# Kernel optimization log

Hardware: AMD Instinct MI355X
Metric: run time of the kernel (lower is better)

The kernel has to match this reference:

```python
import jax, jax.numpy as jnp
import numpy as np


def setup_inputs() -> dict:
    key = jax.random.key(0)
    k_x, k_w, k_s, k_b = jax.random.split(key, 4)
    B, S, D_IN, D_OUT = 8, 2048, 4096, 4096
    x = jax.random.normal(k_x, (B, S, D_IN), dtype=jnp.float32)
    # int8-valued weights stored as int32 (values in [-128, 127])
    quantized_weights = jax.random.randint(k_w, (D_OUT, D_IN), -128, 128, dtype=jnp.int32)
    scales = jax.random.normal(k_s, (D_OUT,), dtype=jnp.float32)
    bias = jax.random.normal(k_b, (D_OUT,), dtype=jnp.float32)
    return {"x": x, "quantized_weights": quantized_weights, "scales": scales, "bias": bias}


def reference(x, quantized_weights, scales, bias):
    # Per-output-channel dequant: W[o, i] = q[o, i] * scales[o]
    dequantized_weight = quantized_weights.astype(x.dtype) * scales[:, None].astype(x.dtype)
    # F.linear: y = x @ W^T + b
    return jnp.einsum('bsi,oi->bso', x, dequantized_weight) + bias.astype(x.dtype)
```

## Files before the change

kernel.cpp:

```cpp
#include <hip/hip_runtime.h>

#define M_DIM 16384
#define N_DIM 4096
#define K_DIM 4096
#define NT 32

typedef __attribute__((ext_vector_type(4))) float f32x4;
typedef __attribute__((ext_vector_type(8))) short bf16x8;
typedef __attribute__((ext_vector_type(4))) int i32x4;

__device__ __forceinline__ short f2bf(float f) {
    unsigned int u = __builtin_bit_cast(unsigned int, f);
    u += 0x7FFFu + ((u >> 16) & 1u);
    return (short)(u >> 16);
}

__global__ __launch_bounds__(256)
void quant_x_kernel(const float* __restrict__ x, char* __restrict__ x8,
                    float* __restrict__ rs) {
    const int row = blockIdx.x;
    const int tid = threadIdx.x;
    const float* xr = x + (size_t)row * K_DIM;
    f32x4 v[4];
    float am = 0.f;
#pragma unroll
    for (int p = 0; p < 4; ++p) {
        v[p] = *(const f32x4*)(xr + p * 1024 + tid * 4);
#pragma unroll
        for (int e = 0; e < 4; ++e) am = fmaxf(am, fabsf(v[p][e]));
    }
#pragma unroll
    for (int off = 32; off >= 1; off >>= 1)
        am = fmaxf(am, __shfl_xor(am, off, 64));
    __shared__ float smax[4];
    if ((tid & 63) == 0) smax[tid >> 6] = am;
    __syncthreads();
    am = fmaxf(fmaxf(smax[0], smax[1]), fmaxf(smax[2], smax[3]));
    const float inv = am > 0.f ? 127.f / am : 0.f;
    if (tid == 0) rs[row] = am / 127.f;
    int* o32 = (int*)(x8 + (size_t)row * K_DIM);
#pragma unroll
    for (int p = 0; p < 4; ++p) {
        const int b0 = (int)rintf(v[p][0] * inv);
        const int b1 = (int)rintf(v[p][1] * inv);
        const int b2 = (int)rintf(v[p][2] * inv);
        const int b3 = (int)rintf(v[p][3] * inv);
        o32[p * 256 + tid] = (b0 & 255) | ((b1 & 255) << 8) | ((b2 & 255) << 16) | ((b3 & 255) << 24);
    }
}

__global__ void quant_w_kernel(const int* __restrict__ q, char* __restrict__ w8, long n) {
    long i = ((long)blockIdx.x * blockDim.x + threadIdx.x) * 16;
    const long stride = (long)gridDim.x * blockDim.x * 16;
    for (; i < n; i += stride) {
        i32x4 o;
#pragma unroll
        for (int j = 0; j < 4; ++j) {
            i32x4 a = *(const i32x4*)(q + i + j * 4);
            o[j] = (a[0] & 255) | ((a[1] & 255) << 8) | ((a[2] & 255) << 16) | ((a[3] & 255) << 24);
        }
        *(i32x4*)(w8 + i) = o;
    }
}

__device__ __forceinline__ void load_lds16(const void* g, void* l) {
    __builtin_amdgcn_global_load_lds((const __attribute__((address_space(1))) void*)g,
                                     (__attribute__((address_space(3))) void*)l, 16, 0, 0);
}

#define BAR() __builtin_amdgcn_s_barrier()
#define VM(n) asm volatile("s_waitcnt vmcnt(" #n ")" ::: "memory")

__global__ __launch_bounds__(512, 2)
void gemm8p_i8(const char* __restrict__ A, const char* __restrict__ Bw,
               const float* __restrict__ rs, const float* __restrict__ scales,
               const float* __restrict__ bias, float* __restrict__ out) {
    __shared__ char lds[2][4][128 * 128];

    const int tid  = threadIdx.x;
    const int lane = tid & 63;
    const int w    = tid >> 6;
    const int wm   = w >> 2;
    const int wn   = w & 3;
    const int lrow = lane & 15;
    const int lkg  = lane >> 4;
    const int sx   = lane & 7;

    const int nwg = gridDim.x;
    const int swz = (blockIdx.x & 7) * (nwg >> 3) + (blockIdx.x >> 3);
    const int bn  = (swz & 15) * 256;
    const int bm  = (swz >> 4) * 256;

    const char* aS[2];
    const char* bS[2];
#pragma unroll
    for (int L = 0; L < 2; ++L) {
        const int c   = L * 512 + tid;
        const int row = c >> 3;
        const int kc  = (c & 7) ^ (row & 7);
        const int mA  = bm + ((row >> 6) << 7) + (row & 63);
        const int nB  = bn + ((row >> 5) << 6) + (row & 31);
        aS[L] = A  + (size_t)mA * K_DIM + kc * 16;
        bS[L] = Bw + (size_t)nB * K_DIM + kc * 16;
    }
    const int wofs = w << 10;

#define STAGE_A(buf, q, kt) do { \
    char* d = &lds[buf][q][wofs]; \
    const long ko = (long)(kt) * 128 + (long)(q) * (64 * (long)K_DIM); \
    load_lds16(aS[0] + ko, d); \
    load_lds16(aS[1] + ko, d + 8192); \
} while (0)

#define STAGE_B(buf, nh, kt) do { \
    char* d = &lds[buf][2 + (nh)][wofs]; \
    const long ko = (long)(kt) * 128 + (long)(nh) * (32 * (long)K_DIM); \
    load_lds16(bS[0] + ko, d); \
    load_lds16(bS[1] + ko, d + 8192); \
} while (0)

    const int aoff = (wm << 6) + lrow;
    const int boff = (wn << 5) + lrow;

#define RD_A(buf, q, sub, ks) \
    (*(const i32x4*)&lds[buf][q][((aoff + (sub) * 16) << 7) + (((((ks) << 2) + lkg) ^ sx) << 4)])
#define RD_B(buf, nh, sub, ks) \
    (*(const i32x4*)&lds[buf][2 + (nh)][((boff + (sub) * 16) << 7) + (((((ks) << 2) + lkg) ^ sx) << 4)])

    i32x4 acc[8][4];
#pragma unroll
    for (int i = 0; i < 8; ++i)
#pragma unroll
        for (int j = 0; j < 4; ++j)
            acc[i][j] = (i32x4){0, 0, 0, 0};

    i32x4 aF[4][2], bF0[2][2], bF1[2][2];

#define LOAD_AF(buf, q) do { \
    _Pragma("unroll") for (int ii = 0; ii < 4; ++ii) { \
        aF[ii][0] = RD_A(buf, q, ii, 0); aF[ii][1] = RD_A(buf, q, ii, 1); } \
} while (0)
#define LOAD_BF(dst, buf, nh) do { \
    _Pragma("unroll") for (int jj = 0; jj < 2; ++jj) { \
        dst[jj][0] = RD_B(buf, nh, jj, 0); dst[jj][1] = RD_B(buf, nh, jj, 1); } \
} while (0)
#define MMA_Q(mh, nh, BREG) do { \
    __builtin_amdgcn_s_setprio(1); \
    _Pragma("unroll") for (int ii = 0; ii < 4; ++ii) \
    _Pragma("unroll") for (int jj = 0; jj < 2; ++jj) \
    _Pragma("unroll") for (int ks = 0; ks < 2; ++ks) \
        acc[(mh) * 4 + ii][(nh) * 2 + jj] = __builtin_amdgcn_mfma_i32_16x16x64_i8( \
            aF[ii][ks], BREG[jj][ks], acc[(mh) * 4 + ii][(nh) * 2 + jj], 0, 0, 0); \
    __builtin_amdgcn_s_setprio(0); \
} while (0)

    STAGE_A(0, 0, 0); STAGE_A(0, 1, 0); STAGE_B(0, 0, 0); STAGE_B(0, 1, 0);
    STAGE_A(1, 0, 1); STAGE_B(1, 0, 1); STAGE_B(1, 1, 1);
    VM(6);
    BAR();

    for (int it = 0; it < NT / 2; ++it) {
        const int kt  = it * 2;
        const bool s2 = (kt + 2 < NT);
        const bool s3 = (kt + 3 < NT);

        LOAD_AF(0, 0); LOAD_BF(bF0, 0, 0);
        STAGE_A(1, 1, kt + 1);
        BAR(); MMA_Q(0, 0, bF0); BAR();
        LOAD_BF(bF1, 0, 1);
        if (s2) STAGE_A(0, 0, kt + 2);
        BAR(); MMA_Q(0, 1, bF1); BAR();
        LOAD_AF(0, 1);
        if (s2) STAGE_B(0, 0, kt + 2);
        BAR(); MMA_Q(1, 0, bF0); BAR();
        if (s2) { STAGE_B(0, 1, kt + 2); VM(6); } else { VM(0); }
        BAR(); MMA_Q(1, 1, bF1); BAR();
        LOAD_AF(1, 0); LOAD_BF(bF0, 1, 0);
        if (s2) STAGE_A(0, 1, kt + 2);
        BAR(); MMA_Q(0, 0, bF0); BAR();
        LOAD_BF(bF1, 1, 1);
        if (s3) STAGE_A(1, 0, kt + 3);
        BAR(); MMA_Q(0, 1, bF1); BAR();
        LOAD_AF(1, 1);
        if (s3) STAGE_B(1, 0, kt + 3);
        BAR(); MMA_Q(1, 0, bF0); BAR();
        if (s3) { STAGE_B(1, 1, kt + 3); VM(6); }
        BAR(); MMA_Q(1, 1, bF1); BAR();
    }

#pragma unroll
    for (int i = 0; i < 8; ++i) {
        const int r0 = bm + (wm << 7) + i * 16 + (lkg << 2);
        const f32x4 rsv = *(const f32x4*)&rs[r0];
#pragma unroll
        for (int j = 0; j < 4; ++j) {
            const int col = bn + (wn << 6) + j * 16 + lrow;
            const float sc = scales[col];
            const float bb = bias[col];
#pragma unroll
            for (int r = 0; r < 4; ++r)
                out[(size_t)(r0 + r) * N_DIM + col] = (float)acc[i][j][r] * (rsv[r] * sc) + bb;
        }
    }
#undef STAGE_A
#undef STAGE_B
#undef RD_A
#undef RD_B
#undef LOAD_AF
#undef LOAD_BF
#undef MMA_Q
}

__global__ __launch_bounds__(256)
void gemm_fallback(const float* __restrict__ Xf, const int* __restrict__ Qw,
                   const float* __restrict__ scales, const float* __restrict__ bias,
                   float* __restrict__ out) {
    __shared__ short a_lds[128 * 64];
    __shared__ short b_lds[128 * 64];
    const int tid  = threadIdx.x;
    const int lane = tid & 63;
    const int wid  = tid >> 6;
    const int wm   = wid >> 1;
    const int wn   = wid & 1;
    const int bn = (blockIdx.x % (N_DIM / 128)) * 128;
    const int bm = (blockIdx.x / (N_DIM / 128)) * 128;
    const int lrow = lane & 15;
    const int lkg  = lane >> 4;

    f32x4 acc[4][4];
#pragma unroll
    for (int i = 0; i < 4; ++i)
#pragma unroll
        for (int j = 0; j < 4; ++j)
            acc[i][j] = (f32x4){0.f, 0.f, 0.f, 0.f};

    for (int k0 = 0; k0 < K_DIM; k0 += 64) {
#pragma unroll
        for (int t = 0; t < 4; ++t) {
            const int ch  = t * 256 + tid;
            const int row = ch >> 3;
            const int kc  = (ch & 7) ^ (row & 7);
            {
                const float* sa = Xf + (size_t)(bm + row) * K_DIM + k0 + kc * 8;
                f32x4 a0 = *(const f32x4*)sa;
                f32x4 a1 = *(const f32x4*)(sa + 4);
                bf16x8 r;
                r[0] = f2bf(a0[0]); r[1] = f2bf(a0[1]); r[2] = f2bf(a0[2]); r[3] = f2bf(a0[3]);
                r[4] = f2bf(a1[0]); r[5] = f2bf(a1[1]); r[6] = f2bf(a1[2]); r[7] = f2bf(a1[3]);
                *(bf16x8*)&a_lds[ch * 8] = r;
            }
            {
                const int* sb = Qw + (size_t)(bn + row) * K_DIM + k0 + kc * 8;
                i32x4 q0 = *(const i32x4*)sb;
                i32x4 q1 = *(const i32x4*)(sb + 4);
                bf16x8 r;
                r[0] = f2bf((float)q0[0]); r[1] = f2bf((float)q0[1]);
                r[2] = f2bf((float)q0[2]); r[3] = f2bf((float)q0[3]);
                r[4] = f2bf((float)q1[0]); r[5] = f2bf((float)q1[1]);
                r[6] = f2bf((float)q1[2]); r[7] = f2bf((float)q1[3]);
                *(bf16x8*)&b_lds[ch * 8] = r;
            }
        }
        __syncthreads();
#pragma unroll
        for (int ks = 0; ks < 2; ++ks) {
            const int kgl = ks * 4 + lkg;
            bf16x8 af[4], bfr[4];
#pragma unroll
            for (int i = 0; i < 4; ++i) {
                const int am = wm * 64 + i * 16 + lrow;
                af[i]  = *(const bf16x8*)&a_lds[am * 64 + ((kgl ^ (am & 7)) << 3)];
                const int bnn = wn * 64 + i * 16 + lrow;
                bfr[i] = *(const bf16x8*)&b_lds[bnn * 64 + ((kgl ^ (bnn & 7)) << 3)];
            }
#pragma unroll
            for (int i = 0; i < 4; ++i)
#pragma unroll
                for (int j = 0; j < 4; ++j)
                    acc[i][j] = __builtin_amdgcn_mfma_f32_16x16x32_bf16(af[i], bfr[j], acc[i][j], 0, 0, 0);
        }
        __syncthreads();
    }
#pragma unroll
    for (int j = 0; j < 4; ++j) {
        const int col = bn + wn * 64 + j * 16 + lrow;
        const float s  = scales[col];
        const float bb = bias[col];
#pragma unroll
        for (int i = 0; i < 4; ++i) {
            const int row0 = bm + wm * 64 + i * 16 + lkg * 4;
#pragma unroll
            for (int r = 0; r < 4; ++r)
                out[(size_t)(row0 + r) * N_DIM + col] = acc[i][j][r] * s + bb;
        }
    }
}

extern "C" void kernel_launch(void* const* d_in, const int* in_sizes, int n_in,
                              void* d_out, int out_size, void* d_ws, size_t ws_size,
                              hipStream_t stream) {
    const float* x      = (const float*)d_in[0];
    const int*   qw     = (const int*)d_in[1];
    const float* scales = (const float*)d_in[2];
    const float* bias   = (const float*)d_in[3];
    float* out = (float*)d_out;

    const size_t x_elems = (size_t)M_DIM * K_DIM;
    const size_t w_elems = (size_t)N_DIM * K_DIM;
    const size_t need    = x_elems + w_elems + M_DIM * sizeof(float);

    if (ws_size >= need) {
        char*  x8 = (char*)d_ws;
        char*  w8 = x8 + x_elems;
        float* rs = (float*)(w8 + w_elems);
        quant_x_kernel<<<M_DIM, 256, 0, stream>>>(x, x8, rs);
        quant_w_kernel<<<2048, 256, 0, stream>>>(qw, w8, (long)w_elems);
        const dim3 grid((M_DIM / 256) * (N_DIM / 256));
        gemm8p_i8<<<grid, 512, 0, stream>>>(x8, w8, rs, scales, bias, out);
    } else {
        const dim3 grid((M_DIM / 128) * (N_DIM / 128));
        gemm_fallback<<<grid, 256, 0, stream>>>(x, qw, scales, bias, out);
    }
}
```

Baseline: 344.7 us.

## Switch int8 GEMM to 32x32x32 MFMA, fuse quant kernels, LDS-staged epilogue

Replaces the 16x16x64 int8 MFMA tiling with 32x32x32 MFMA fragments, which reorganises the LDS read pattern and the accumulator layout. The main loop is peeled so the final iteration has no conditional staging. The output epilogue now goes through LDS scratch so each thread writes coalesced float4 stores with vectorised scale and bias loads. The two quantisation kernels are merged into one launch to save a kernel launch. The risks are extra LDS round-trips in the epilogue and different register pressure from the larger accumulators.

New measurement: 381.9 us. +10.8%, slower.

```diff
diff --git a/kernel.cpp b/kernel.cpp
--- a/kernel.cpp
+++ b/kernel.cpp
@@ -5,9 +5,10 @@
 #define K_DIM 4096
 #define NT 32
 
-typedef __attribute__((ext_vector_type(4))) float f32x4;
-typedef __attribute__((ext_vector_type(8))) short bf16x8;
-typedef __attribute__((ext_vector_type(4))) int i32x4;
+typedef __attribute__((ext_vector_type(4)))  float f32x4;
+typedef __attribute__((ext_vector_type(8)))  short bf16x8;
+typedef __attribute__((ext_vector_type(4)))  int   i32x4;
+typedef __attribute__((ext_vector_type(16))) int   i32x16;
 
 __device__ __forceinline__ short f2bf(float f) {
     unsigned int u = __builtin_bit_cast(unsigned int, f);
@@ -16,50 +17,52 @@
 }
 
 __global__ __launch_bounds__(256)
-void quant_x_kernel(const float* __restrict__ x, char* __restrict__ x8,
-                    float* __restrict__ rs) {
-    const int row = blockIdx.x;
+void quant_kernel(const float* __restrict__ x, const int* __restrict__ q,
+                  char* __restrict__ x8, char* __restrict__ w8,
+                  float* __restrict__ rs) {
     const int tid = threadIdx.x;
-    const float* xr = x + (size_t)row * K_DIM;
-    f32x4 v[4];
-    float am = 0.f;
-#pragma unroll
-    for (int p = 0; p < 4; ++p) {
-        v[p] = *(const f32x4*)(xr + p * 1024 + tid * 4);
-#pragma unroll
-        for (int e = 0; e < 4; ++e) am = fmaxf(am, fabsf(v[p][e]));
-    }
-#pragma unroll
-    for (int off = 32; off >= 1; off >>= 1)
-        am = fmaxf(am, __shfl_xor(am, off, 64));
-    __shared__ float smax[4];
-    if ((tid & 63) == 0) smax[tid >> 6] = am;
-    __syncthreads();
-    am = fmaxf(fmaxf(smax[0], smax[1]), fmaxf(smax[2], smax[3]));
-    const float inv = am > 0.f ? 127.f / am : 0.f;
-    if (tid == 0) rs[row] = am / 127.f;
-    int* o32 = (int*)(x8 + (size_t)row * K_DIM);
-#pragma unroll
-    for (int p = 0; p < 4; ++p) {
-        const int b0 = (int)rintf(v[p][0] * inv);
-        const int b1 = (int)rintf(v[p][1] * inv);
-        const int b2 = (int)rintf(v[p][2] * inv);
-        const int b3 = (int)rintf(v[p][3] * inv);
-        o32[p * 256 + tid] = (b0 & 255) | ((b1 & 255) << 8) | ((b2 & 255) << 16) | ((b3 & 255) << 24);
-    }
-}
-
-__global__ void quant_w_kernel(const int* __restrict__ q, char* __restrict__ w8, long n) {
-    long i = ((long)blockIdx.x * blockDim.x + threadIdx.x) * 16;
-    const long stride = (long)gridDim.x * blockDim.x * 16;
-    for (; i < n; i += stride) {
-        i32x4 o;
-#pragma unroll
-        for (int j = 0; j < 4; ++j) {
-            i32x4 a = *(const i32x4*)(q + i + j * 4);
-            o[j] = (a[0] & 255) | ((a[1] & 255) << 8) | ((a[2] & 255) << 16) | ((a[3] & 255) << 24);
-        }
-        *(i32x4*)(w8 + i) = o;
+    if (blockIdx.x < M_DIM) {
+        const int row = blockIdx.x;
+        const float* xr = x + (size_t)row * K_DIM;
+        f32x4 v[4];
+        float am = 0.f;
+#pragma unroll
+        for (int p = 0; p < 4; ++p) {
+            v[p] = *(const f32x4*)(xr + p * 1024 + tid * 4);
+#pragma unroll
+            for (int e = 0; e < 4; ++e) am = fmaxf(am, fabsf(v[p][e]));
+        }
+#pragma unroll
+        for (int off = 32; off >= 1; off >>= 1)
+            am = fmaxf(am, __shfl_xor(am, off, 64));
+        __shared__ float smax[4];
+        if ((tid & 63) == 0) smax[tid >> 6] = am;
+        __syncthreads();
+        am = fmaxf(fmaxf(smax[0], smax[1]), fmaxf(smax[2], smax[3]));
+        const float inv = am > 0.f ? 127.f / am : 0.f;
+        if (tid == 0) rs[row] = am / 127.f;
+        int* o32 = (int*)(x8 + (size_t)row * K_DIM);
+#pragma unroll
+        for (int p = 0; p < 4; ++p) {
+            const int b0 = (int)rintf(v[p][0] * inv);
+            const int b1 = (int)rintf(v[p][1] * inv);
+            const int b2 = (int)rintf(v[p][2] * inv);
+            const int b3 = (int)rintf(v[p][3] * inv);
+            o32[p * 256 + tid] = (b0 & 255) | ((b1 & 255) << 8) | ((b2 & 255) << 16) | ((b3 & 255) << 24);
+        }
+    } else {
+        const long n = (long)N_DIM * K_DIM;
+        long i = ((long)(blockIdx.x - M_DIM) * 256 + tid) * 16;
+        const long stride = 2048L * 256 * 16;
+        for (; i < n; i += stride) {
+            i32x4 o;
+#pragma unroll
+            for (int j = 0; j < 4; ++j) {
+                i32x4 a = *(const i32x4*)(q + i + j * 4);
+                o[j] = (a[0] & 255) | ((a[1] & 255) << 8) | ((a[2] & 255) << 16) | ((a[3] & 255) << 24);
+            }
+            *(i32x4*)(w8 + i) = o;
+        }
     }
 }
 
@@ -82,8 +85,8 @@
     const int w    = tid >> 6;
     const int wm   = w >> 2;
     const int wn   = w & 3;
-    const int lrow = lane & 15;
-    const int lkg  = lane >> 4;
+    const int l31  = lane & 31;
+    const int kg   = lane >> 5;
     const int sx   = lane & 7;
 
     const int nwg = gridDim.x;
@@ -119,39 +122,52 @@
     load_lds16(bS[1] + ko, d + 8192); \
 } while (0)
 
-    const int aoff = (wm << 6) + lrow;
-    const int boff = (wn << 5) + lrow;
-
-#define RD_A(buf, q, sub, ks) \
-    (*(const i32x4*)&lds[buf][q][((aoff + (sub) * 16) << 7) + (((((ks) << 2) + lkg) ^ sx) << 4)])
-#define RD_B(buf, nh, sub, ks) \
-    (*(const i32x4*)&lds[buf][2 + (nh)][((boff + (sub) * 16) << 7) + (((((ks) << 2) + lkg) ^ sx) << 4)])
-
-    i32x4 acc[8][4];
-#pragma unroll
-    for (int i = 0; i < 8; ++i)
-#pragma unroll
-        for (int j = 0; j < 4; ++j)
-            acc[i][j] = (i32x4){0, 0, 0, 0};
-
-    i32x4 aF[4][2], bF0[2][2], bF1[2][2];
+#define RD_A(buf, q, mf, ks) \
+    (*(const i32x4*)&lds[buf][q][(((wm << 6) + (mf) * 32 + l31) << 7) + (((((ks) << 1) + kg) ^ sx) << 4)])
+#define RD_B(buf, nh, ks) \
+    (*(const i32x4*)&lds[buf][2 + (nh)][(((wn << 5) + l31) << 7) + (((((ks) << 1) + kg) ^ sx) << 4)])
+
+    i32x16 acc[4][2];
+#pragma unroll
+    for (int i = 0; i < 4; ++i)
+#pragma unroll
+        for (int j = 0; j < 2; ++j)
+#pragma unroll
+            for (int r = 0; r < 16; ++r) acc[i][j][r] = 0;
+
+    i32x4 aF[2][4], bF0[4], bF1[4];
 
 #define LOAD_AF(buf, q) do { \
-    _Pragma("unroll") for (int ii = 0; ii < 4; ++ii) { \
-        aF[ii][0] = RD_A(buf, q, ii, 0); aF[ii][1] = RD_A(buf, q, ii, 1); } \
+    _Pragma("unroll") for (int mf = 0; mf < 2; ++mf) \
+    _Pragma("unroll") for (int ks = 0; ks < 4; ++ks) aF[mf][ks] = RD_A(buf, q, mf, ks); \
 } while (0)
 #define LOAD_BF(dst, buf, nh) do { \
-    _Pragma("unroll") for (int jj = 0; jj < 2; ++jj) { \
-        dst[jj][0] = RD_B(buf, nh, jj, 0); dst[jj][1] = RD_B(buf, nh, jj, 1); } \
-} while (0)
-#define MMA_Q(mh, nh, BREG) do { \
+    _Pragma("unroll") for (int ks = 0; ks < 4; ++ks) dst[ks] = RD_B(buf, nh, ks); \
+} while (0)
+#define MMA_Q(q, nh, BREG) do { \
     __builtin_amdgcn_s_setprio(1); \
-    _Pragma("unroll") for (int ii = 0; ii < 4; ++ii) \
-    _Pragma("unroll") for (int jj = 0; jj < 2; ++jj) \
-    _Pragma("unroll") for (int ks = 0; ks < 2; ++ks) \
-        acc[(mh) * 4 + ii][(nh) * 2 + jj] = __builtin_amdgcn_mfma_i32_16x16x64_i8( \
-            aF[ii][ks], BREG[jj][ks], acc[(mh) * 4 + ii][(nh) * 2 + jj], 0, 0, 0); \
+    _Pragma("unroll") for (int ks = 0; ks < 4; ++ks) \
+    _Pragma("unroll") for (int mf = 0; mf < 2; ++mf) \
+        acc[(q) * 2 + mf][nh] = __builtin_amdgcn_mfma_i32_32x32x32_i8( \
+            aF[mf][ks], BREG[ks], acc[(q) * 2 + mf][nh], 0, 0, 0); \
     __builtin_amdgcn_s_setprio(0); \
+} while (0)
+
+#define PHASES(kt, S1, S2, S3, S4, S5, S6, S7, S8, VMA, VMB) do { \
+    LOAD_AF(0, 0); LOAD_BF(bF0, 0, 0); \
+    S1; BAR(); MMA_Q(0, 0, bF0); BAR(); \
+    LOAD_BF(bF1, 0, 1); \
+    S2; BAR(); MMA_Q(0, 1, bF1); BAR(); \
+    LOAD_AF(0, 1); \
+    S3; BAR(); MMA_Q(1, 0, bF0); BAR(); \
+    S4; VMA; BAR(); MMA_Q(1, 1, bF1); BAR(); \
+    LOAD_AF(1, 0); LOAD_BF(bF0, 1, 0); \
+    S5; BAR(); MMA_Q(0, 0, bF0); BAR(); \
+    LOAD_BF(bF1, 1, 1); \
+    S6; BAR(); MMA_Q(0, 1, bF1); BAR(); \
+    LOAD_AF(1, 1); \
+    S7; BAR(); MMA_Q(1, 0, bF0); BAR(); \
+    S8; VMB; BAR(); MMA_Q(1, 1, bF1); BAR(); \
 } while (0)
 
     STAGE_A(0, 0, 0); STAGE_A(0, 1, 0); STAGE_B(0, 0, 0); STAGE_B(0, 1, 0);
@@ -159,47 +175,46 @@
     VM(6);
     BAR();
 
-    for (int it = 0; it < NT / 2; ++it) {
-        const int kt  = it * 2;
-        const bool s2 = (kt + 2 < NT);
-        const bool s3 = (kt + 3 < NT);
-
-        LOAD_AF(0, 0); LOAD_BF(bF0, 0, 0);
-        STAGE_A(1, 1, kt + 1);
-        BAR(); MMA_Q(0, 0, bF0); BAR();
-        LOAD_BF(bF1, 0, 1);
-        if (s2) STAGE_A(0, 0, kt + 2);
-        BAR(); MMA_Q(0, 1, bF1); BAR();
-        LOAD_AF(0, 1);
-        if (s2) STAGE_B(0, 0, kt + 2);
-        BAR(); MMA_Q(1, 0, bF0); BAR();
-        if (s2) { STAGE_B(0, 1, kt + 2); VM(6); } else { VM(0); }
-        BAR(); MMA_Q(1, 1, bF1); BAR();
-        LOAD_AF(1, 0); LOAD_BF(bF0, 1, 0);
-        if (s2) STAGE_A(0, 1, kt + 2);
-        BAR(); MMA_Q(0, 0, bF0); BAR();
-        LOAD_BF(bF1, 1, 1);
-        if (s3) STAGE_A(1, 0, kt + 3);
-        BAR(); MMA_Q(0, 1, bF1); BAR();
-        LOAD_AF(1, 1);
-        if (s3) STAGE_B(1, 0, kt + 3);
-        BAR(); MMA_Q(1, 0, bF0); BAR();
-        if (s3) { STAGE_B(1, 1, kt + 3); VM(6); }
-        BAR(); MMA_Q(1, 1, bF1); BAR();
-    }
-
-#pragma unroll
-    for (int i = 0; i < 8; ++i) {
-        const int r0 = bm + (wm << 7) + i * 16 + (lkg << 2);
-        const f32x4 rsv = *(const f32x4*)&rs[r0];
-#pragma unroll
-        for (int j = 0; j < 4; ++j) {
-            const int col = bn + (wn << 6) + j * 16 + lrow;
-            const float sc = scales[col];
-            const float bb = bias[col];
-#pragma unroll
-            for (int r = 0; r < 4; ++r)
-                out[(size_t)(r0 + r) * N_DIM + col] = (float)acc[i][j][r] * (rsv[r] * sc) + bb;
+    for (int it = 0; it < 15; ++it) {
+        const int kt = it * 2;
+        PHASES(kt,
+               STAGE_A(1, 1, kt + 1),
+               STAGE_A(0, 0, kt + 2),
+               STAGE_B(0, 0, kt + 2),
+               STAGE_B(0, 1, kt + 2),
+               STAGE_A(0, 1, kt + 2),
+               STAGE_A(1, 0, kt + 3),
+               STAGE_B(1, 0, kt + 3),
+               STAGE_B(1, 1, kt + 3),
+               VM(6), VM(6));
+    }
+    PHASES(30, STAGE_A(1, 1, 31), , , , , , , , VM(0), );
+
+    float* scratch = (float*)(&lds[0][0][0]) + w * 1024;
+#pragma unroll
+    for (int mfg = 0; mfg < 4; ++mfg) {
+        const int gr0 = bm + (wm << 7) + mfg * 32;
+#pragma unroll
+        for (int nf = 0; nf < 2; ++nf) {
+            const int gc0 = bn + (wn << 6) + nf * 32;
+#pragma unroll
+            for (int r = 0; r < 16; ++r) {
+                const int row = (r & 3) + ((r >> 2) << 3) + (kg << 2);
+                scratch[row * 32 + l31] = (float)acc[mfg][nf][r];
+            }
+            const int colq = (lane & 7) * 4;
+            const f32x4 sc = *(const f32x4*)&scales[gc0 + colq];
+            const f32x4 bb = *(const f32x4*)&bias[gc0 + colq];
+#pragma unroll
+            for (int s = 0; s < 4; ++s) {
+                const int row_l = s * 8 + (lane >> 3);
+                f32x4 v = *(const f32x4*)&scratch[row_l * 32 + colq];
+                const float rsv = rs[gr0 + row_l];
+                f32x4 o;
+#pragma unroll
+                for (int e = 0; e < 4; ++e) o[e] = v[e] * (rsv * sc[e]) + bb[e];
+                *(f32x4*)&out[(size_t)(gr0 + row_l) * N_DIM + gc0 + colq] = o;
+            }
         }
     }
 #undef STAGE_A
@@ -209,6 +224,7 @@
 #undef LOAD_AF
 #undef LOAD_BF
 #undef MMA_Q
+#undef PHASES
 }
 
 __global__ __launch_bounds__(256)
@@ -313,8 +329,7 @@
         char*  x8 = (char*)d_ws;
         char*  w8 = x8 + x_elems;
         float* rs = (float*)(w8 + w_elems);
-        quant_x_kernel<<<M_DIM, 256, 0, stream>>>(x, x8, rs);
-        quant_w_kernel<<<2048, 256, 0, stream>>>(qw, w8, (long)w_elems);
+        quant_kernel<<<M_DIM + 2048, 256, 0, stream>>>(x, qw, x8, w8, rs);
         const dim3 grid((M_DIM / 256) * (N_DIM / 256));
         gemm8p_i8<<<grid, 512, 0, stream>>>(x8, w8, rs, scales, bias, out);
     } else {
```
